# Performance work log

Hardware: AMD Instinct MI355X
Metric: run time of the kernel (lower is better)

## Reference

```python
import jax, jax.numpy as jnp
import numpy as np

H = 16        # num_attention_heads
D = 128       # head_dim
HID = 2048    # hidden_size
S = 2048      # seq_len
B = 2
EPS = 1.1920928955078125e-07  # torch.finfo(float32).eps, F.rms_norm default


def _rope(x, cos, sin):
    # x: [B,H,S,D]; cos/sin: [S, D//2] broadcast over B,H
    d = x.shape[-1] // 2
    x1, x2 = x[..., :d], x[..., d:]
    return jnp.concatenate([x1 * cos + x2 * sin, -x1 * sin + x2 * cos], axis=-1)


def _rmsnorm(x):
    ms = jnp.mean(x * x, axis=-1, keepdims=True)
    return x * jax.lax.rsqrt(ms + EPS)


def setup_inputs() -> dict:
    key = jax.random.key(0)
    ks = jax.random.split(key, 7)
    x = jax.random.normal(ks[0], (B, S, HID), dtype=jnp.float32)
    cos = jax.random.uniform(ks[1], (S, D // 2), dtype=jnp.float32)
    sin = jax.random.uniform(ks[2], (S, D // 2), dtype=jnp.float32)
    sc = 1.0 / np.sqrt(HID)
    wq = jax.random.normal(ks[3], (H * D, HID), dtype=jnp.float32) * sc
    wk = jax.random.normal(ks[4], (D, HID), dtype=jnp.float32) * sc  # num_kv_heads=1
    wv = jax.random.normal(ks[5], (D, HID), dtype=jnp.float32) * sc
    wo = jax.random.normal(ks[6], (HID, H * D), dtype=jnp.float32) * sc
    return {"x": x, "cos": cos, "sin": sin, "wq": wq, "wk": wk, "wv": wv, "wo": wo}


def reference(x, cos, sin, wq, wk, wv, wo):
    b, s, _ = x.shape
    # projections
    q = (x @ wq.T).reshape(b, s, H, D).transpose(0, 2, 1, 3)        # [b,H,s,D]
    k = (x @ wk.T).reshape(b, s, 1, D).transpose(0, 2, 1, 3)        # [b,1,s,D] MQA
    v = (x @ wv.T).reshape(b, s, 1, D).transpose(0, 2, 1, 3)
    # RoPE then RMS-norm on q/k (keep k/v in MQA [b,1,s,D]; broadcasting replaces expand)
    q = _rmsnorm(_rope(q, cos, sin))
    k = _rmsnorm(_rope(k, cos, sin))
    # causal attention
    scores = jnp.einsum('bhqd,bgkd->bhqk', q, k) * (D ** -0.5)      # [b,H,s,s]
    mask = jnp.tril(jnp.ones((s, s), dtype=bool))
    scores = jnp.where(mask, scores, -jnp.inf)
    attn = jax.nn.softmax(scores, axis=-1)
    out = jnp.einsum('bhqk,bgkd->bhqd', attn, v)                    # [b,H,s,D]
    out = out.transpose(0, 2, 1, 3).reshape(b, s, H * D)
    return out @ wo.T
```

## Files before the change

kernel.cpp:

```cpp
#include <hip/hip_runtime.h>
#include <hip/hip_bf16.h>

typedef __attribute__((ext_vector_type(8))) short bf16x8;
typedef __attribute__((ext_vector_type(4))) short bf16x4;
typedef __attribute__((ext_vector_type(4))) float f32x4;

constexpr int cH = 16, cD = 128, cHID = 2048, cS = 2048, cB = 2;
constexpr float cEPS = 1.1920928955078125e-07f;
constexpr float cQS = 0.08838834764831845f * 1.442695040888963f;

__device__ __forceinline__ unsigned short f2bf(float f) {
  union { float f; unsigned u; } v; v.f = f;
  unsigned r = v.u + 0x7fffu + ((v.u >> 16) & 1u);
  return (unsigned short)(r >> 16);
}
__device__ __forceinline__ unsigned pk2(float a, float b) {
  return (unsigned)f2bf(a) | ((unsigned)f2bf(b) << 16);
}
__device__ __forceinline__ unsigned cvtpk(float a, float b) {
  unsigned r;
  asm("v_cvt_pk_bf16_f32 %0, %1, %2" : "=v"(r) : "v"(a), "v"(b));
  return r;
}
__device__ __forceinline__ f32x4 mfma16(bf16x8 a, bf16x8 b, f32x4 c) {
  return __builtin_amdgcn_mfma_f32_16x16x32_bf16(a, b, c, 0, 0, 0);
}
__device__ __forceinline__ f32x4 mfma16k16(bf16x4 a, bf16x4 b, f32x4 c) {
#if __has_builtin(__builtin_amdgcn_mfma_f32_16x16x16bf16_1k)
  return __builtin_amdgcn_mfma_f32_16x16x16bf16_1k(a, b, c, 0, 0, 0);
#else
  f32x4 d;
  asm volatile("v_mfma_f32_16x16x16_bf16 %0, %1, %2, %3\n\ts_nop 7\n\ts_nop 2"
               : "=v"(d) : "v"(a), "v"(b), "v"(c));
  return d;
#endif
}
__device__ __forceinline__ void gl2l(const void* g, void* l) {
  __builtin_amdgcn_global_load_lds(
      (const __attribute__((address_space(1))) unsigned int*)g,
      (__attribute__((address_space(3))) unsigned int*)l, 16, 0, 0);
}

__global__ __launch_bounds__(256) void cvt_all(
    const float* __restrict__ x, const float* __restrict__ wq,
    const float* __restrict__ wk, const float* __restrict__ wv,
    const float* __restrict__ wo,
    unsigned short* __restrict__ xb, unsigned short* __restrict__ wqb,
    unsigned short* __restrict__ wkb, unsigned short* __restrict__ wvb,
    unsigned short* __restrict__ wob)
{
  long i = (long)blockIdx.x * 2048 + threadIdx.x * 8;
  const float* s; unsigned short* d; long off;
  if (i < 8388608)       { s = x;  d = xb;  off = i; }
  else if (i < 12582912) { s = wq; d = wqb; off = i - 8388608; }
  else if (i < 12845056) { s = wk; d = wkb; off = i - 12582912; }
  else if (i < 13107200) { s = wv; d = wvb; off = i - 12845056; }
  else                   { s = wo; d = wob; off = i - 13107200; }
  float4 v0 = *reinterpret_cast<const float4*>(s + off);
  float4 v1 = *reinterpret_cast<const float4*>(s + off + 4);
  uint4 o; o.x = pk2(v0.x, v0.y); o.y = pk2(v0.z, v0.w);
  o.z = pk2(v1.x, v1.y); o.w = pk2(v1.z, v1.w);
  *reinterpret_cast<uint4*>(d + off) = o;
}

__global__ __launch_bounds__(256) void gemm_qkv(
    const unsigned short* __restrict__ A,
    const unsigned short* __restrict__ Wq,
    const unsigned short* __restrict__ Wk,
    const unsigned short* __restrict__ Wv,
    const float* __restrict__ cosb, const float* __restrict__ sinb,
    unsigned short* __restrict__ Qn,
    unsigned short* __restrict__ Kn,
    unsigned short* __restrict__ Vn)
{
  __shared__ unsigned short lds[8192];
  const int t = threadIdx.x;
  const int bm = blockIdx.x, bn = blockIdx.y;
  const int lane = t & 63, w = t >> 6;
  const int hi = lane >> 4, l15 = lane & 15;

  const unsigned short* Wp; long wbase;
  if (bn < 16)       { Wp = Wq; wbase = (long)bn * 128; }
  else if (bn == 16) { Wp = Wk; wbase = 0; }
  else               { Wp = Wv; wbase = 0; }

  f32x4 acc[2][8] = {};

  for (int k0 = 0; k0 < 2048; k0 += 32) {
    #pragma unroll
    for (int i = 0; i < 2; ++i) {
      int c = w + 4 * i;
      gl2l(A + (long)(bm * 128 + 16 * c + (lane >> 2)) * 2048 + k0 + (lane & 3) * 8,
           &lds[c * 512]);
      gl2l(Wp + (wbase + 16 * c + (lane >> 2)) * 2048 + k0 + (lane & 3) * 8,
           &lds[4096 + c * 512]);
    }
    __syncthreads();
    bf16x8 af[2], bff[8];
    #pragma unroll
    for (int m = 0; m < 2; ++m)
      af[m] = *reinterpret_cast<const bf16x8*>(&lds[(w * 32 + m * 16 + l15) * 32 + hi * 8]);
    #pragma unroll
    for (int n = 0; n < 8; ++n)
      bff[n] = *reinterpret_cast<const bf16x8*>(&lds[4096 + (n * 16 + l15) * 32 + hi * 8]);
    #pragma unroll
    for (int m = 0; m < 2; ++m)
      #pragma unroll
      for (int n = 0; n < 8; ++n)
        acc[m][n] = mfma16(af[m], bff[n], acc[m][n]);
    __syncthreads();
  }

  const int rowbase = bm * 128 + w * 32;
  if (bn == 17) {
    #pragma unroll
    for (int m = 0; m < 2; ++m)
      #pragma unroll
      for (int r = 0; r < 4; ++r) {
        int grow = rowbase + m * 16 + hi * 4 + r;
        int b = grow >> 11, s = grow & 2047;
        long base = ((long)b * cS + s) * cD;
        #pragma unroll
        for (int n = 0; n < 8; ++n)
          Vn[base + n * 16 + l15] = f2bf(acc[m][n][r]);
      }
  } else {
    #pragma unroll
    for (int m = 0; m < 2; ++m)
      #pragma unroll
      for (int r = 0; r < 4; ++r) {
        int grow = rowbase + m * 16 + hi * 4 + r;
        int b = grow >> 11, s = grow & 2047;
        float o1[4], o2[4], ss = 0.f;
        #pragma unroll
        for (int n = 0; n < 4; ++n) {
          float cv = cosb[(long)s * 64 + n * 16 + l15];
          float sv = sinb[(long)s * 64 + n * 16 + l15];
          float x1 = acc[m][n][r], x2 = acc[m][n + 4][r];
          o1[n] = x1 * cv + x2 * sv;
          o2[n] = x2 * cv - x1 * sv;
          ss += o1[n] * o1[n] + o2[n] * o2[n];
        }
        ss += __shfl_xor(ss, 1); ss += __shfl_xor(ss, 2);
        ss += __shfl_xor(ss, 4); ss += __shfl_xor(ss, 8);
        float scn = rsqrtf(ss * (1.0f / 128.0f) + cEPS);
        if (bn < 16) {
          float sq = scn * cQS;
          long base = (((long)b * cH + bn) * cS + s) * cD;
          #pragma unroll
          for (int n = 0; n < 4; ++n) {
            Qn[base + n * 16 + l15] = f2bf(o1[n] * sq);
            Qn[base + 64 + n * 16 + l15] = f2bf(o2[n] * sq);
          }
        } else {
          long base = ((long)b * cS + s) * cD;
          int xs = (s & 7) << 3;
          #pragma unroll
          for (int n = 0; n < 4; ++n) {
            Kn[base + ((n * 16 + l15) ^ xs)] = f2bf(o1[n] * scn);
            Kn[base + (((64 + n * 16 + l15)) ^ xs)] = f2bf(o2[n] * scn);
          }
        }
      }
  }
}

__global__ __launch_bounds__(256) void vtrans(
    const unsigned short* __restrict__ Vn, unsigned short* __restrict__ Vt)
{
  __shared__ unsigned short Tl[64][72];
  const int t = threadIdx.x;
  const int st = blockIdx.x * 64, dt = blockIdx.y * 64, b = blockIdx.z;
  const unsigned short* Vb = Vn + (long)b * cS * cD;
  #pragma unroll
  for (int i = 0; i < 2; ++i) {
    int r = i * 32 + (t >> 3), c8 = (t & 7) * 8;
    *reinterpret_cast<uint4*>(&Tl[r][c8]) =
        *reinterpret_cast<const uint4*>(&Vb[(long)(st + r) * cD + dt + c8]);
  }
  __syncthreads();
  unsigned short* Vo = Vt + (long)b * cD * cS;
  #pragma unroll
  for (int i = 0; i < 2; ++i) {
    int d = i * 32 + (t >> 3), sb = (t & 7) * 8;
    unsigned short e[8];
    #pragma unroll
    for (int j = 0; j < 8; ++j) e[j] = Tl[sb + j][d];
    uint4 o;
    o.x = (unsigned)e[0] | ((unsigned)e[1] << 16);
    o.y = (unsigned)e[2] | ((unsigned)e[3] << 16);
    o.z = (unsigned)e[4] | ((unsigned)e[5] << 16);
    o.w = (unsigned)e[6] | ((unsigned)e[7] << 16);
    int dg = dt + d;
    *reinterpret_cast<uint4*>(&Vo[(long)dg * cS + st + (sb ^ ((dg & 7) << 3))]) = o;
  }
}

__global__ __launch_bounds__(256) void attn2(
    const unsigned short* __restrict__ Qn,
    const unsigned short* __restrict__ Kn,
    const unsigned short* __restrict__ Vt,
    unsigned short* __restrict__ O)
{
  __shared__ unsigned short lds[32768];
  const int t = threadIdx.x, w = t >> 6, lane = t & 63;
  const int hi = lane >> 4, l15 = lane & 15;
  const int h = blockIdx.y, b = blockIdx.z;
  const unsigned short* Qb = Qn + (long)(b * cH + h) * cS * cD;
  const unsigned short* Kb = Kn + (long)b * cS * cD;
  const unsigned short* Vtb = Vt + (long)b * cD * cS;
  const int x3 = (l15 & 7) << 3;

  union O4 { unsigned u[2]; bf16x4 v; };
  O4 o4; o4.u[0] = o4.u[1] = 0x3F803F80u;
  const bf16x4 ones4 = o4.v;

  #pragma unroll 1
  for (int pass = 0; pass < 2; ++pass) {
    const int qt = (pass == 0) ? blockIdx.x : 31 - blockIdx.x;
    const int q0 = qt * 64;
    const int qrow = q0 + w * 16 + l15;
    const int nt = qt + 1;

    bf16x8 qf[4];
    #pragma unroll
    for (int kc = 0; kc < 4; ++kc)
      qf[kc] = *reinterpret_cast<const bf16x8*>(&Qb[(long)qrow * cD + kc * 32 + hi * 8]);

    const unsigned short* kp = Kb + (long)(16 * w + (lane >> 4)) * cD + (lane & 15) * 8;
    const unsigned short* vp[4];
    #pragma unroll
    for (int i = 0; i < 4; ++i)
      vp[i] = Vtb + (long)(32 * w + 8 * i + (lane >> 3)) * cS + (lane & 7) * 8;

    auto STAGE = [&](int buf) {
      unsigned short* kd = &lds[buf * 8192 + w * 2048];
      unsigned short* vd = &lds[16384 + buf * 8192 + w * 2048];
      #pragma unroll
      for (int i = 0; i < 4; ++i) {
        gl2l(kp + i * 512, kd + i * 512);
        gl2l(vp[i], vd + i * 512);
      }
      kp += 8192;
      #pragma unroll
      for (int i = 0; i < 4; ++i) vp[i] += 64;
    };

    f32x4 oacc[8] = {};
    f32x4 lacc = {};
    float mrun = -1e30f;

    STAGE(0);
    int cur = 0;

    #pragma unroll 1
    for (int kt = 0; kt < nt; ++kt) {
      const int kv0 = kt * 64;
      if (kt + 1 < nt) {
        STAGE(cur ^ 1);
        asm volatile("s_waitcnt vmcnt(8)" ::: "memory");
      } else {
        asm volatile("s_waitcnt vmcnt(0)" ::: "memory");
      }
      __builtin_amdgcn_s_barrier();
      __builtin_amdgcn_sched_barrier(0);

      const unsigned short* kbase = &lds[cur * 8192];
      const unsigned short* vbase = &lds[16384 + cur * 8192];

      f32x4 st[4] = {};
      __builtin_amdgcn_s_setprio(1);
      #pragma unroll
      for (int kc = 0; kc < 4; ++kc) {
        #pragma unroll
        for (int n = 0; n < 4; ++n) {
          bf16x8 kf = *reinterpret_cast<const bf16x8*>(
              &kbase[(n * 16 + l15) * 128 + ((kc * 32 + hi * 8) ^ x3)]);
          st[n] = mfma16(kf, qf[kc], st[n]);
        }
      }
      __builtin_amdgcn_s_setprio(0);

      float p[4][4];
      if (kt == qt) {
        #pragma unroll
        for (int n = 0; n < 4; ++n)
          #pragma unroll
          for (int r = 0; r < 4; ++r) {
            int kv = kv0 + n * 16 + hi * 4 + r;
            p[n][r] = (kv <= qrow) ? st[n][r] : -1e30f;
          }
      } else {
        #pragma unroll
        for (int n = 0; n < 4; ++n)
          #pragma unroll
          for (int r = 0; r < 4; ++r)
            p[n][r] = st[n][r];
      }

      float t0 = fmaxf(fmaxf(p[0][0], p[0][1]), fmaxf(p[0][2], p[0][3]));
      float t1 = fmaxf(fmaxf(p[1][0], p[1][1]), fmaxf(p[1][2], p[1][3]));
      float t2 = fmaxf(fmaxf(p[2][0], p[2][1]), fmaxf(p[2][2], p[2][3]));
      float t3 = fmaxf(fmaxf(p[3][0], p[3][1]), fmaxf(p[3][2], p[3][3]));
      float pmax = fmaxf(fmaxf(t0, t1), fmaxf(t2, t3));

      if (!__all(pmax - mrun <= 8.0f)) {
        pmax = fmaxf(pmax, __shfl_xor(pmax, 16));
        pmax = fmaxf(pmax, __shfl_xor(pmax, 32));
        float mnew = fmaxf(mrun, pmax);
        float alpha = exp2f(mrun - mnew);
        mrun = mnew;
        #pragma unroll
        for (int n = 0; n < 8; ++n)
          #pragma unroll
          for (int r = 0; r < 4; ++r) oacc[n][r] *= alpha;
        #pragma unroll
        for (int r = 0; r < 4; ++r) lacc[r] *= alpha;
      }

      #pragma unroll
      for (int n = 0; n < 4; ++n)
        #pragma unroll
        for (int r = 0; r < 4; ++r)
          p[n][r] = exp2f(p[n][r] - mrun);

      bf16x4 paB[4];
      #pragma unroll
      for (int n = 0; n < 4; ++n) {
        O4 pu;
        pu.u[0] = cvtpk(p[n][0], p[n][1]);
        pu.u[1] = cvtpk(p[n][2], p[n][3]);
        paB[n] = pu.v;
      }

      __builtin_amdgcn_s_setprio(1);
      #pragma unroll
      for (int n = 0; n < 4; ++n) lacc = mfma16k16(ones4, paB[n], lacc);
      #pragma unroll
      for (int n2 = 0; n2 < 8; ++n2) {
        #pragma unroll
        for (int n = 0; n < 4; ++n) {
          bf16x4 vf = *reinterpret_cast<const bf16x4*>(
              &vbase[(n2 * 16 + l15) * 64 + ((n * 16 + hi * 4) ^ x3)]);
          oacc[n2] = mfma16k16(vf, paB[n], oacc[n2]);
        }
      }
      __builtin_amdgcn_s_setprio(0);
      __builtin_amdgcn_s_barrier();
      cur ^= 1;
    }

    {
      float inv = 1.0f / lacc[0];
      unsigned short* Ol = &lds[w * 2176];
      #pragma unroll
      for (int n2 = 0; n2 < 8; ++n2)
        #pragma unroll
        for (int r = 0; r < 4; ++r)
          Ol[l15 * 136 + n2 * 16 + hi * 4 + r] = f2bf(oacc[n2][r] * inv);
      __syncthreads();
      #pragma unroll
      for (int i = 0; i < 4; ++i) {
        int row = hi + 4 * i;
        uint4 ov = *reinterpret_cast<const uint4*>(&Ol[row * 136 + l15 * 8]);
        *reinterpret_cast<uint4*>(
            &O[(long)(b * cS + q0 + w * 16 + row) * (cH * cD) + h * cD + l15 * 8]) = ov;
      }
      __syncthreads();
    }
  }
}

__global__ __launch_bounds__(256) void gemm_out(
    const unsigned short* __restrict__ A,
    const unsigned short* __restrict__ W,
    float* __restrict__ C)
{
  __shared__ unsigned short lds[8192];
  const int t = threadIdx.x;
  const int bm = blockIdx.x, bn = blockIdx.y;
  const int lane = t & 63, w = t >> 6;
  const int wr = w >> 1, wc = w & 1, hi = lane >> 4, l15 = lane & 15;
  const long wbase = (long)bn * 128;

  f32x4 acc[4][4] = {};
  for (int k0 = 0; k0 < 2048; k0 += 32) {
    #pragma unroll
    for (int i = 0; i < 2; ++i) {
      int c = w + 4 * i;
      gl2l(A + (long)(bm * 128 + 16 * c + (lane >> 2)) * 2048 + k0 + (lane & 3) * 8,
           &lds[c * 512]);
      gl2l(W + (wbase + 16 * c + (lane >> 2)) * 2048 + k0 + (lane & 3) * 8,
           &lds[4096 + c * 512]);
    }
    __syncthreads();
    bf16x8 af[4], bff[4];
    #pragma unroll
    for (int m = 0; m < 4; ++m)
      af[m] = *reinterpret_cast<const bf16x8*>(&lds[(wr * 64 + m * 16 + l15) * 32 + hi * 8]);
    #pragma unroll
    for (int n = 0; n < 4; ++n)
      bff[n] = *reinterpret_cast<const bf16x8*>(&lds[4096 + (wc * 64 + n * 16 + l15) * 32 + hi * 8]);
    #pragma unroll
    for (int m = 0; m < 4; ++m)
      #pragma unroll
      for (int n = 0; n < 4; ++n)
        acc[m][n] = mfma16(af[m], bff[n], acc[m][n]);
    __syncthreads();
  }

  #pragma unroll
  for (int m = 0; m < 4; ++m) {
    int row = bm * 128 + wr * 64 + m * 16 + hi * 4;
    #pragma unroll
    for (int n = 0; n < 4; ++n) {
      int col = bn * 128 + wc * 64 + n * 16 + l15;
      #pragma unroll
      for (int r = 0; r < 4; ++r)
        C[(long)(row + r) * 2048 + col] = acc[m][n][r];
    }
  }
}

extern "C" void kernel_launch(void* const* d_in, const int* in_sizes, int n_in,
                              void* d_out, int out_size, void* d_ws, size_t ws_size,
                              hipStream_t stream) {
  const float* x    = (const float*)d_in[0];
  const float* cosb = (const float*)d_in[1];
  const float* sinb = (const float*)d_in[2];
  const float* wq   = (const float*)d_in[3];
  const float* wk   = (const float*)d_in[4];
  const float* wv   = (const float*)d_in[5];
  const float* wo   = (const float*)d_in[6];
  float* out = (float*)d_out;

  char* ws = (char*)d_ws;
  unsigned short* xb  = (unsigned short*)(ws);
  unsigned short* wqb = (unsigned short*)(ws + 16777216);
  unsigned short* wkb = (unsigned short*)(ws + 25165824);
  unsigned short* wvb = (unsigned short*)(ws + 25690112);
  unsigned short* Qn  = (unsigned short*)(ws + 26214400);
  unsigned short* Kn  = (unsigned short*)(ws + 42991616);
  unsigned short* Vn  = (unsigned short*)(ws + 44040192);
  unsigned short* Vtg = (unsigned short*)(ws + 45088768);
  unsigned short* wob = (unsigned short*)(ws + 46137344);
  unsigned short* Ob  = (unsigned short*)ws;

  cvt_all<<<dim3(8448), 256, 0, stream>>>(x, wq, wk, wv, wo, xb, wqb, wkb, wvb, wob);
  gemm_qkv<<<dim3(32, 18), 256, 0, stream>>>(xb, wqb, wkb, wvb, cosb, sinb, Qn, Kn, Vn);
  vtrans<<<dim3(32, 2, 2), 256, 0, stream>>>(Vn, Vtg);
  attn2<<<dim3(16, 16, 2), 256, 0, stream>>>(Qn, Kn, Vtg, Ob);
  gemm_out<<<dim3(32, 16), 256, 0, stream>>>(Ob, wob, out);
}
```

Before: 204.2 us.

## Process two 16-row query tiles per wave to reuse staged K/V

Each attention block now covers 128 query rows instead of 64, with each wave holding two 16-row Q fragments. Every K/V fragment read from LDS then feeds two MFMA chains, which halves the K/V global and LDS traffic per query row and doubles MFMA work per load. The grid is halved and the causal pass pairing is adjusted to match. In exchange, accumulator registers roughly double, which can lower occupancy, and the wider diagonal tiles compute more scores that are masked out.

```diff
diff --git a/kernel.cpp b/kernel.cpp
--- a/kernel.cpp
+++ b/kernel.cpp
@@ -217,15 +217,18 @@
 
   #pragma unroll 1
   for (int pass = 0; pass < 2; ++pass) {
-    const int qt = (pass == 0) ? blockIdx.x : 31 - blockIdx.x;
-    const int q0 = qt * 64;
-    const int qrow = q0 + w * 16 + l15;
-    const int nt = qt + 1;
-
-    bf16x8 qf[4];
-    #pragma unroll
-    for (int kc = 0; kc < 4; ++kc)
-      qf[kc] = *reinterpret_cast<const bf16x8*>(&Qb[(long)qrow * cD + kc * 32 + hi * 8]);
+    const int qt = (pass == 0) ? blockIdx.x : 15 - blockIdx.x;
+    const int q0 = qt * 128 + w * 32;
+    const int qrowA = q0 + l15;
+    const int qrowB = q0 + 16 + l15;
+    const int nt = 2 * qt + 2;
+
+    bf16x8 qfA[4], qfB[4];
+    #pragma unroll
+    for (int kc = 0; kc < 4; ++kc) {
+      qfA[kc] = *reinterpret_cast<const bf16x8*>(&Qb[(long)qrowA * cD + kc * 32 + hi * 8]);
+      qfB[kc] = *reinterpret_cast<const bf16x8*>(&Qb[(long)qrowB * cD + kc * 32 + hi * 8]);
+    }
 
     const unsigned short* kp = Kb + (long)(16 * w + (lane >> 4)) * cD + (lane & 15) * 8;
     const unsigned short* vp[4];
@@ -246,12 +249,62 @@
       for (int i = 0; i < 4; ++i) vp[i] += 64;
     };
 
-    f32x4 oacc[8] = {};
-    f32x4 lacc = {};
-    float mrun = -1e30f;
+    f32x4 oaccA[8] = {}, oaccB[8] = {};
+    f32x4 laccA = {}, laccB = {};
+    float mrunA = -1e30f, mrunB = -1e30f;
 
     STAGE(0);
     int cur = 0;
+
+    auto SOFTMAX = [&](f32x4 (&st)[4], float& mrun, f32x4& lacc, f32x4 (&oacc)[8],
+                       bf16x4 (&paOut)[4], int qrow, int kv0, bool domask) {
+      float p[4][4];
+      if (domask) {
+        #pragma unroll
+        for (int n = 0; n < 4; ++n)
+          #pragma unroll
+          for (int r = 0; r < 4; ++r) {
+            int kv = kv0 + n * 16 + hi * 4 + r;
+            p[n][r] = (kv <= qrow) ? st[n][r] : -1e30f;
+          }
+      } else {
+        #pragma unroll
+        for (int n = 0; n < 4; ++n)
+          #pragma unroll
+          for (int r = 0; r < 4; ++r)
+            p[n][r] = st[n][r];
+      }
+      float t0 = fmaxf(fmaxf(p[0][0], p[0][1]), fmaxf(p[0][2], p[0][3]));
+      float t1 = fmaxf(fmaxf(p[1][0], p[1][1]), fmaxf(p[1][2], p[1][3]));
+      float t2 = fmaxf(fmaxf(p[2][0], p[2][1]), fmaxf(p[2][2], p[2][3]));
+      float t3 = fmaxf(fmaxf(p[3][0], p[3][1]), fmaxf(p[3][2], p[3][3]));
+      float pmax = fmaxf(fmaxf(t0, t1), fmaxf(t2, t3));
+      if (!__all(pmax - mrun <= 8.0f)) {
+        pmax = fmaxf(pmax, __shfl_xor(pmax, 16));
+        pmax = fmaxf(pmax, __shfl_xor(pmax, 32));
+        float mnew = fmaxf(mrun, pmax);
+        float alpha = exp2f(mrun - mnew);
+        mrun = mnew;
+        #pragma unroll
+        for (int n = 0; n < 8; ++n)
+          #pragma unroll
+          for (int r = 0; r < 4; ++r) oacc[n][r] *= alpha;
+        #pragma unroll
+        for (int r = 0; r < 4; ++r) lacc[r] *= alpha;
+      }
+      #pragma unroll
+      for (int n = 0; n < 4; ++n)
+        #pragma unroll
+        for (int r = 0; r < 4; ++r)
+          p[n][r] = exp2f(p[n][r] - mrun);
+      #pragma unroll
+      for (int n = 0; n < 4; ++n) {
+        O4 pu;
+        pu.u[0] = cvtpk(p[n][0], p[n][1]);
+        pu.u[1] = cvtpk(p[n][2], p[n][3]);
+        paOut[n] = pu.v;
+      }
+    };
 
     #pragma unroll 1
     for (int kt = 0; kt < nt; ++kt) {
@@ -268,7 +321,7 @@
       const unsigned short* kbase = &lds[cur * 8192];
       const unsigned short* vbase = &lds[16384 + cur * 8192];
 
-      f32x4 st[4] = {};
+      f32x4 stA[4] = {}, stB[4] = {};
       __builtin_amdgcn_s_setprio(1);
       #pragma unroll
       for (int kc = 0; kc < 4; ++kc) {
@@ -276,73 +329,31 @@
         for (int n = 0; n < 4; ++n) {
           bf16x8 kf = *reinterpret_cast<const bf16x8*>(
               &kbase[(n * 16 + l15) * 128 + ((kc * 32 + hi * 8) ^ x3)]);
-          st[n] = mfma16(kf, qf[kc], st[n]);
+          stA[n] = mfma16(kf, qfA[kc], stA[n]);
+          stB[n] = mfma16(kf, qfB[kc], stB[n]);
         }
       }
       __builtin_amdgcn_s_setprio(0);
 
-      float p[4][4];
-      if (kt == qt) {
-        #pragma unroll
-        for (int n = 0; n < 4; ++n)
-          #pragma unroll
-          for (int r = 0; r < 4; ++r) {
-            int kv = kv0 + n * 16 + hi * 4 + r;
-            p[n][r] = (kv <= qrow) ? st[n][r] : -1e30f;
-          }
-      } else {
-        #pragma unroll
-        for (int n = 0; n < 4; ++n)
-          #pragma unroll
-          for (int r = 0; r < 4; ++r)
-            p[n][r] = st[n][r];
-      }
-
-      float t0 = fmaxf(fmaxf(p[0][0], p[0][1]), fmaxf(p[0][2], p[0][3]));
-      float t1 = fmaxf(fmaxf(p[1][0], p[1][1]), fmaxf(p[1][2], p[1][3]));
-      float t2 = fmaxf(fmaxf(p[2][0], p[2][1]), fmaxf(p[2][2], p[2][3]));
-      float t3 = fmaxf(fmaxf(p[3][0], p[3][1]), fmaxf(p[3][2], p[3][3]));
-      float pmax = fmaxf(fmaxf(t0, t1), fmaxf(t2, t3));
-
-      if (!__all(pmax - mrun <= 8.0f)) {
-        pmax = fmaxf(pmax, __shfl_xor(pmax, 16));
-        pmax = fmaxf(pmax, __shfl_xor(pmax, 32));
-        float mnew = fmaxf(mrun, pmax);
-        float alpha = exp2f(mrun - mnew);
-        mrun = mnew;
-        #pragma unroll
-        for (int n = 0; n < 8; ++n)
-          #pragma unroll
-          for (int r = 0; r < 4; ++r) oacc[n][r] *= alpha;
-        #pragma unroll
-        for (int r = 0; r < 4; ++r) lacc[r] *= alpha;
-      }
-
-      #pragma unroll
-      for (int n = 0; n < 4; ++n)
-        #pragma unroll
-        for (int r = 0; r < 4; ++r)
-          p[n][r] = exp2f(p[n][r] - mrun);
-
-      bf16x4 paB[4];
+      const bool domask = (kt >= 2 * qt);
+      bf16x4 paA[4], paB[4];
+      SOFTMAX(stA, mrunA, laccA, oaccA, paA, qrowA, kv0, domask);
+      SOFTMAX(stB, mrunB, laccB, oaccB, paB, qrowB, kv0, domask);
+
+      __builtin_amdgcn_s_setprio(1);
       #pragma unroll
       for (int n = 0; n < 4; ++n) {
-        O4 pu;
-        pu.u[0] = cvtpk(p[n][0], p[n][1]);
-        pu.u[1] = cvtpk(p[n][2], p[n][3]);
-        paB[n] = pu.v;
-      }
-
-      __builtin_amdgcn_s_setprio(1);
-      #pragma unroll
-      for (int n = 0; n < 4; ++n) lacc = mfma16k16(ones4, paB[n], lacc);
+        laccA = mfma16k16(ones4, paA[n], laccA);
+        laccB = mfma16k16(ones4, paB[n], laccB);
+      }
       #pragma unroll
       for (int n2 = 0; n2 < 8; ++n2) {
         #pragma unroll
         for (int n = 0; n < 4; ++n) {
           bf16x4 vf = *reinterpret_cast<const bf16x4*>(
               &vbase[(n2 * 16 + l15) * 64 + ((n * 16 + hi * 4) ^ x3)]);
-          oacc[n2] = mfma16k16(vf, paB[n], oacc[n2]);
+          oaccA[n2] = mfma16k16(vf, paA[n], oaccA[n2]);
+          oaccB[n2] = mfma16k16(vf, paB[n], oaccB[n2]);
         }
       }
       __builtin_amdgcn_s_setprio(0);
@@ -350,8 +361,12 @@
       cur ^= 1;
     }
 
-    {
+    #pragma unroll
+    for (int half = 0; half < 2; ++half) {
+      f32x4& lacc = half ? laccB : laccA;
+      f32x4* oacc = half ? oaccB : oaccA;
       float inv = 1.0f / lacc[0];
+      int qb = q0 + half * 16;
       unsigned short* Ol = &lds[w * 2176];
       #pragma unroll
       for (int n2 = 0; n2 < 8; ++n2)
@@ -364,7 +379,7 @@
         int row = hi + 4 * i;
         uint4 ov = *reinterpret_cast<const uint4*>(&Ol[row * 136 + l15 * 8]);
         *reinterpret_cast<uint4*>(
-            &O[(long)(b * cS + q0 + w * 16 + row) * (cH * cD) + h * cD + l15 * 8]) = ov;
+            &O[(long)(b * cS + qb + row) * (cH * cD) + h * cD + l15 * 8]) = ov;
       }
       __syncthreads();
     }
@@ -449,6 +464,6 @@
   cvt_all<<<dim3(8448), 256, 0, stream>>>(x, wq, wk, wv, wo, xb, wqb, wkb, wvb, wob);
   gemm_qkv<<<dim3(32, 18), 256, 0, stream>>>(xb, wqb, wkb, wvb, cosb, sinb, Qn, Kn, Vn);
   vtrans<<<dim3(32, 2, 2), 256, 0, stream>>>(Vn, Vtg);
-  attn2<<<dim3(16, 16, 2), 256, 0, stream>>>(Qn, Kn, Vtg, Ob);
+  attn2<<<dim3(8, 16, 2), 256, 0, stream>>>(Qn, Kn, Vtg, Ob);
   gemm_out<<<dim3(32, 16), 256, 0, stream>>>(Ob, wob, out);
 }
```

Result: slower. 217.0 us (+6.3%).
